# Kernel optimization log

Measured on AMD Instinct MI355X. Metric: run time of the kernel, lower is better.

## Reference

```python
import jax, jax.numpy as jnp
import numpy as np

N = 50000      # nodes
E = 800000     # edges (avg degree 16)
IN = 128       # in_channels
H = 8          # heads (layer 1)
C = 32         # hidden_channels per head
OUT = 40       # out_channels + 1
NEG_SLOPE = 0.2  # PyG GATConv default


def glorot(key, shape, fan_in, fan_out):
    lim = np.sqrt(6.0 / (fan_in + fan_out)).astype(np.float32)
    return jax.random.uniform(key, shape, jnp.float32, -lim, lim)


def setup_inputs() -> dict:
    key = jax.random.key(0)
    ks = jax.random.split(key, 10)
    x = jax.random.normal(ks[0], (N, IN), jnp.float32)
    edge_index = jax.random.randint(ks[1], (2, E), 0, N, dtype=jnp.int32)
    # layer 1: in -> H*C, heads=8, concat
    W1 = glorot(ks[2], (IN, H * C), IN, H * C)
    att_src1 = glorot(ks[3], (H, C), C, C)
    att_dst1 = glorot(ks[4], (H, C), C, C)
    b1 = jnp.zeros((H * C,), jnp.float32)
    # layer 2: H*C -> OUT, heads=1
    W2 = glorot(ks[5], (H * C, OUT), H * C, OUT)
    att_src2 = glorot(ks[6], (1, OUT), OUT, OUT)
    att_dst2 = glorot(ks[7], (1, OUT), OUT, OUT)
    b2 = jnp.zeros((OUT,), jnp.float32)
    return {"x": x, "edge_index": edge_index, "W1": W1, "att_src1": att_src1,
            "att_dst1": att_dst1, "b1": b1, "W2": W2, "att_src2": att_src2,
            "att_dst2": att_dst2, "b2": b2}


def gat_conv(x, edge_index, W, att_src, att_dst, bias):
    # PyG GATConv (eval mode, add_self_loops=True, concat=True)
    n = x.shape[0]
    heads, ch = att_src.shape
    loop = jnp.arange(n, dtype=edge_index.dtype)
    src = jnp.concatenate([edge_index[0], loop])  # message source j
    dst = jnp.concatenate([edge_index[1], loop])  # message target i
    h = (x @ W).reshape(n, heads, ch)                       # [N,H,C]
    a_src = jnp.einsum('nhc,hc->nh', h, att_src)            # [N,H]
    a_dst = jnp.einsum('nhc,hc->nh', h, att_dst)            # [N,H]
    logits = jax.nn.leaky_relu(a_src[src] + a_dst[dst], NEG_SLOPE)  # [Et,H]
    # segmented softmax over incoming edges of each target node
    m = jax.ops.segment_max(logits, dst, num_segments=n)    # [N,H]
    p = jnp.exp(logits - m[dst])
    s = jax.ops.segment_sum(p, dst, num_segments=n)         # [N,H]
    alpha = p / s[dst]                                      # [Et,H]
    msg = h[src] * alpha[:, :, None]                        # [Et,H,C]
    out = jax.ops.segment_sum(msg, dst, num_segments=n)     # [N,H,C]
    return out.reshape(n, heads * ch) + bias


def reference(x, edge_index, W1, att_src1, att_dst1, b1, W2, att_src2, att_dst2, b2):
    h = gat_conv(x, edge_index, W1, att_src1, att_dst1, b1)
    h = jax.nn.relu(h)  # dropout is identity in eval mode
    h = gat_conv(h, edge_index, W2, att_src2, att_dst2, b2)
    return jax.nn.log_softmax(h, axis=1)
```

## Files before the change

kernel.cpp:

```cpp
#include <hip/hip_runtime.h>
#include <hip/hip_bf16.h>
#include <math.h>

#define NEG_SLOPE 0.2f

__device__ __forceinline__ float lrelu(float x){ return x > 0.f ? x : NEG_SLOPE * x; }
__device__ __forceinline__ unsigned short f2bf(float f){
  __hip_bfloat16 h = __float2bfloat16(f);
  return __builtin_bit_cast(unsigned short, h);
}
__device__ __forceinline__ float b2f(unsigned short u){
  return __builtin_bit_cast(float, (unsigned)u << 16);
}

typedef short bf16x8 __attribute__((ext_vector_type(8)));
typedef float f32x4 __attribute__((ext_vector_type(4)));

__global__ void k_count(const int* __restrict__ dst, int* __restrict__ deg, int E){
  int e = blockIdx.x*256 + threadIdx.x;
  if (e < E) atomicAdd(&deg[dst[e]], 1);
}

__global__ __launch_bounds__(256) void k_scan1(const int* __restrict__ deg, int* __restrict__ bsum, int n){
  int tid = threadIdx.x;
  int base = blockIdx.x*1024 + tid*4;
  int s = 0;
  #pragma unroll
  for (int j=0;j<4;j++){ int idx = base+j; if (idx < n) s += deg[idx]; }
  #pragma unroll
  for (int off=32; off; off>>=1) s += __shfl_xor(s, off);
  __shared__ int ws[4];
  if ((tid&63)==0) ws[tid>>6] = s;
  __syncthreads();
  if (tid==0) bsum[blockIdx.x] = ws[0]+ws[1]+ws[2]+ws[3];
}

__global__ void k_scan2(const int* __restrict__ bsum, int* __restrict__ boff,
                        int* __restrict__ rowptr, int nb, int n){
  int lane = threadIdx.x;
  int v = (lane < nb) ? bsum[lane] : 0;
  int inc = v;
  #pragma unroll
  for (int off=1; off<64; off<<=1){ int t = __shfl_up(inc, off); if (lane >= off) inc += t; }
  if (lane < nb) boff[lane] = inc - v;
  if (lane == 63) rowptr[n] = inc;
}

__global__ __launch_bounds__(256) void k_scan3(const int* __restrict__ deg, const int* __restrict__ boff,
    int* __restrict__ rowptr, int* __restrict__ nxt, int n){
  int tid = threadIdx.x; int lane = tid & 63, w = tid >> 6;
  int base = blockIdx.x*1024 + tid*4;
  int v[4]; int s = 0;
  #pragma unroll
  for (int j=0;j<4;j++){ int idx = base+j; v[j] = (idx < n) ? deg[idx] : 0; s += v[j]; }
  int inc = s;
  #pragma unroll
  for (int off=1; off<64; off<<=1){ int t = __shfl_up(inc, off); if (lane >= off) inc += t; }
  __shared__ int ws[4];
  if (lane == 63) ws[w] = inc;
  __syncthreads();
  int run = boff[blockIdx.x];
  for (int ww=0; ww<w; ww++) run += ws[ww];
  run += inc - s;
  #pragma unroll
  for (int j=0;j<4;j++){ int idx = base+j; if (idx < n){ rowptr[idx] = run; nxt[idx] = run; run += v[j]; } }
}

__global__ void k_scatter(const int* __restrict__ src, const int* __restrict__ dst,
                          int* __restrict__ nxt, int* __restrict__ srcs,
                          int* __restrict__ dsts, int E){
  int e = blockIdx.x*256 + threadIdx.x;
  if (e < E){
    int d = dst[e];
    int pos = atomicAdd(&nxt[d], 1);
    srcs[pos] = src[e];
    dsts[pos] = d;
  }
}

__global__ void k_wt(const float* __restrict__ W, unsigned short* __restrict__ Wt, int NCreal){
  int c = blockIdx.x, k = threadIdx.x, K = blockDim.x;
  float v = (c < NCreal) ? W[(size_t)k*NCreal + c] : 0.f;
  Wt[(size_t)c*K + k] = f2bf(v);
}

__global__ void k_edgep1(const int* __restrict__ srcs, const int* __restrict__ dsts,
    const float* __restrict__ asrc, const float* __restrict__ adst,
    unsigned short* __restrict__ p1, int E8){
  int id = blockIdx.x*256 + threadIdx.x;
  if (id >= E8) return;
  int pos = id >> 3, hd = id & 7;
  int s = srcs[pos], d = dsts[pos];
  float l = lrelu(asrc[(size_t)s*8 + hd] + adst[(size_t)d*8 + hd]);
  p1[id] = f2bf(__expf(l));
}

__global__ void k_edgep2(const int* __restrict__ srcs, const int* __restrict__ dsts,
    const float* __restrict__ asrc, const float* __restrict__ adst,
    float* __restrict__ p2, int E){
  int pos = blockIdx.x*256 + threadIdx.x;
  if (pos >= E) return;
  int s = srcs[pos], d = dsts[pos];
  p2[pos] = __expf(lrelu(asrc[s] + adst[d]));
}

__global__ __launch_bounds__(256) void gemm1_att(
    const float* __restrict__ x, const unsigned short* __restrict__ Bt,
    unsigned short* __restrict__ C, const float* __restrict__ att_s,
    const float* __restrict__ att_d, float* __restrict__ asrc,
    float* __restrict__ adst, int M){
  __shared__ unsigned short sA[64][40];
  __shared__ unsigned short sB[256][40];
  const int tid = threadIdx.x;
  const int wid = tid >> 6, lane = tid & 63;
  const int r0 = blockIdx.x * 64;
  const int fr = lane & 15, fk = (lane >> 4) * 8;
  f32x4 acc[4][4] = {};

  for (int k0 = 0; k0 < 128; k0 += 32){
    #pragma unroll
    for (int t=0; t<2; t++){
      int id = tid + t*256;
      int r = id >> 3, q = id & 7;
      float4 v = make_float4(0.f,0.f,0.f,0.f);
      int row = r0 + r;
      if (row < M) v = ((const float4*)(x + (size_t)row*128))[(k0>>2) + q];
      ushort4 o; o.x=f2bf(v.x); o.y=f2bf(v.y); o.z=f2bf(v.z); o.w=f2bf(v.w);
      *(ushort4*)&sA[r][q*4] = o;
    }
    #pragma unroll
    for (int t=0; t<4; t++){
      int id = tid + t*256;
      int r = id >> 2, lk = (id & 3) * 8;
      uint4 vb = *(const uint4*)(Bt + (size_t)r*128 + k0 + lk);
      *(uint4*)&sB[r][lk] = vb;
    }
    __syncthreads();
    bf16x8 a[4], b[4];
    #pragma unroll
    for (int mi=0; mi<4; mi++) a[mi] = *(const bf16x8*)&sA[mi*16 + fr][fk];
    #pragma unroll
    for (int ni=0; ni<4; ni++) b[ni] = *(const bf16x8*)&sB[wid*64 + ni*16 + fr][fk];
    #pragma unroll
    for (int mi=0; mi<4; mi++)
      #pragma unroll
      for (int ni=0; ni<4; ni++)
        acc[mi][ni] = __builtin_amdgcn_mfma_f32_16x16x32_bf16(a[mi], b[ni], acc[mi][ni], 0,0,0);
    __syncthreads();
  }

  float avs[4], avd[4];
  #pragma unroll
  for (int ni=0; ni<4; ni++){
    int idx = (2*wid + (ni>>1))*32 + (ni&1)*16 + fr;
    avs[ni] = att_s[idx];
    avd[ni] = att_d[idx];
  }

  #pragma unroll
  for (int mi=0; mi<4; mi++){
    #pragma unroll
    for (int j=0; j<4; j++){
      int row = r0 + mi*16 + (lane>>4)*4 + j;
      #pragma unroll
      for (int ni=0; ni<4; ni++){
        int col = wid*64 + ni*16 + fr;
        if (row < M) C[(size_t)row*256 + col] = f2bf(acc[mi][ni][j]);
      }
      float s0 = acc[mi][0][j]*avs[0] + acc[mi][1][j]*avs[1];
      float s1 = acc[mi][2][j]*avs[2] + acc[mi][3][j]*avs[3];
      float d0 = acc[mi][0][j]*avd[0] + acc[mi][1][j]*avd[1];
      float d1 = acc[mi][2][j]*avd[2] + acc[mi][3][j]*avd[3];
      #pragma unroll
      for (int mk=1; mk<16; mk<<=1){
        s0 += __shfl_xor(s0, mk); s1 += __shfl_xor(s1, mk);
        d0 += __shfl_xor(d0, mk); d1 += __shfl_xor(d1, mk);
      }
      if ((lane & 15) == 0 && row < M){
        asrc[(size_t)row*8 + 2*wid    ] = s0;
        asrc[(size_t)row*8 + 2*wid + 1] = s1;
        adst[(size_t)row*8 + 2*wid    ] = d0;
        adst[(size_t)row*8 + 2*wid + 1] = d1;
      }
    }
  }
}

__global__ __launch_bounds__(256) void gemm_mfma(
    const unsigned short* __restrict__ A, const unsigned short* __restrict__ Bt,
    unsigned short* __restrict__ C, int M, int K, int ldc){
  __shared__ unsigned short sA[64][40];
  __shared__ unsigned short sB[64][40];
  const int tid = threadIdx.x;
  const int wid = tid >> 6, lane = tid & 63;
  const int r0 = blockIdx.x * 64, c0 = blockIdx.y * 64;
  const int wr = wid >> 1, wc = wid & 1;
  const int lr = tid >> 2;
  const int lk = (tid & 3) * 8;
  const int fr = lane & 15, fk = (lane >> 4) * 8;
  f32x4 acc[2][2] = {};

  for (int k0 = 0; k0 < K; k0 += 32){
    uint4 va = make_uint4(0,0,0,0);
    int row = r0 + lr;
    if (row < M) va = *(const uint4*)(A + (size_t)row*K + k0 + lk);
    *(uint4*)&sA[lr][lk] = va;
    uint4 vb = *(const uint4*)(Bt + (size_t)(c0 + lr)*K + k0 + lk);
    *(uint4*)&sB[lr][lk] = vb;
    __syncthreads();
    bf16x8 a0 = *(const bf16x8*)&sA[wr*32 + fr][fk];
    bf16x8 a1 = *(const bf16x8*)&sA[wr*32 + 16 + fr][fk];
    bf16x8 b0 = *(const bf16x8*)&sB[wc*32 + fr][fk];
    bf16x8 b1 = *(const bf16x8*)&sB[wc*32 + 16 + fr][fk];
    acc[0][0] = __builtin_amdgcn_mfma_f32_16x16x32_bf16(a0, b0, acc[0][0], 0,0,0);
    acc[0][1] = __builtin_amdgcn_mfma_f32_16x16x32_bf16(a0, b1, acc[0][1], 0,0,0);
    acc[1][0] = __builtin_amdgcn_mfma_f32_16x16x32_bf16(a1, b0, acc[1][0], 0,0,0);
    acc[1][1] = __builtin_amdgcn_mfma_f32_16x16x32_bf16(a1, b1, acc[1][1], 0,0,0);
    __syncthreads();
  }
  #pragma unroll
  for (int mi=0; mi<2; mi++){
    int rowb = r0 + wr*32 + mi*16 + (lane>>4)*4;
    #pragma unroll
    for (int ni=0; ni<2; ni++){
      int col = c0 + wc*32 + ni*16 + fr;
      #pragma unroll
      for (int j=0;j<4;j++){
        int row = rowb + j;
        if (row < M) C[(size_t)row*ldc + col] = f2bf(acc[mi][ni][j]);
      }
    }
  }
}

__global__ void k_att2(const unsigned short* __restrict__ h, const float* __restrict__ att_s,
    const float* __restrict__ att_d, float* __restrict__ asrc, float* __restrict__ adst, int n){
  int id = blockIdx.x*256 + threadIdx.x;
  if (id >= n) return;
  const unsigned short* hv = h + (size_t)id*64;
  float s = 0.f, d = 0.f;
  #pragma unroll
  for (int q=0; q<5; q++){
    ushort4 u0 = ((const ushort4*)hv)[q*2];
    ushort4 u1 = ((const ushort4*)hv)[q*2+1];
    float v0=b2f(u0.x), v1=b2f(u0.y), v2=b2f(u0.z), v3=b2f(u0.w);
    float v4=b2f(u1.x), v5=b2f(u1.y), v6=b2f(u1.z), v7=b2f(u1.w);
    float4 a0 = ((const float4*)att_s)[q*2], a1 = ((const float4*)att_s)[q*2+1];
    float4 d0 = ((const float4*)att_d)[q*2], d1 = ((const float4*)att_d)[q*2+1];
    s += v0*a0.x + v1*a0.y + v2*a0.z + v3*a0.w + v4*a1.x + v5*a1.y + v6*a1.z + v7*a1.w;
    d += v0*d0.x + v1*d0.y + v2*d0.z + v3*d0.w + v4*d1.x + v5*d1.y + v6*d1.z + v7*d1.w;
  }
  asrc[id] = s; adst[id] = d;
}

__global__ __launch_bounds__(256) void k_agg1(
    const unsigned short* __restrict__ h1, const float* __restrict__ asrc,
    const float* __restrict__ adst, const int* __restrict__ rowptr,
    const int* __restrict__ srcs, const unsigned short* __restrict__ p1,
    const float* __restrict__ bias, unsigned short* __restrict__ zb, int n){
  int i = (blockIdx.x*256 + threadIdx.x) >> 6;
  int lane = threadIdx.x & 63;
  if (i >= n) return;
  int hd = lane >> 3;
  float pself = __expf(lrelu(asrc[(size_t)i*8 + hd] + adst[(size_t)i*8 + hd]));
  float ssum = pself;
  uint2 hs = ((const uint2*)(h1 + (size_t)i*256))[lane];
  float4 acc;
  acc.x = pself * b2f((unsigned short)(hs.x & 0xffff));
  acc.y = pself * b2f((unsigned short)(hs.x >> 16));
  acc.z = pself * b2f((unsigned short)(hs.y & 0xffff));
  acc.w = pself * b2f((unsigned short)(hs.y >> 16));
  int e0 = rowptr[i], e1 = rowptr[i+1];
  int efull = e0 + ((e1 - e0) & ~7);
  for (int e = e0; e < efull; e += 8){
    int sx[8]; uint2 vv[8]; float pv[8];
    #pragma unroll
    for (int j=0;j<8;j++) sx[j] = srcs[e+j];
    #pragma unroll
    for (int j=0;j<8;j++) vv[j] = ((const uint2*)(h1 + (size_t)sx[j]*256))[lane];
    #pragma unroll
    for (int j=0;j<8;j++) pv[j] = b2f(p1[(size_t)(e+j)*8 + hd]);
    #pragma unroll
    for (int j=0;j<8;j++){
      float p = pv[j];
      ssum += p;
      acc.x += p * b2f((unsigned short)(vv[j].x & 0xffff));
      acc.y += p * b2f((unsigned short)(vv[j].x >> 16));
      acc.z += p * b2f((unsigned short)(vv[j].y & 0xffff));
      acc.w += p * b2f((unsigned short)(vv[j].y >> 16));
    }
  }
  if (efull < e1){
    int sx[8]; uint2 vv[8]; float pv[8];
    #pragma unroll
    for (int j=0;j<8;j++){
      int ee = efull + j;
      int idx = ee < e1 ? ee : e1 - 1;
      sx[j] = srcs[idx];
      unsigned short pr = p1[(size_t)idx*8 + hd];
      pv[j] = (ee < e1) ? b2f(pr) : 0.f;
    }
    #pragma unroll
    for (int j=0;j<8;j++) vv[j] = ((const uint2*)(h1 + (size_t)sx[j]*256))[lane];
    #pragma unroll
    for (int j=0;j<8;j++){
      float p = pv[j];
      ssum += p;
      acc.x += p * b2f((unsigned short)(vv[j].x & 0xffff));
      acc.y += p * b2f((unsigned short)(vv[j].x >> 16));
      acc.z += p * b2f((unsigned short)(vv[j].y & 0xffff));
      acc.w += p * b2f((unsigned short)(vv[j].y >> 16));
    }
  }
  float inv = 1.f / ssum;
  float4 b = ((const float4*)bias)[lane];
  ushort4 ob;
  ob.x = f2bf(fmaxf(fmaf(acc.x, inv, b.x), 0.f));
  ob.y = f2bf(fmaxf(fmaf(acc.y, inv, b.y), 0.f));
  ob.z = f2bf(fmaxf(fmaf(acc.z, inv, b.z), 0.f));
  ob.w = f2bf(fmaxf(fmaf(acc.w, inv, b.w), 0.f));
  ((ushort4*)(zb + (size_t)i*256))[lane] = ob;
}

__global__ __launch_bounds__(256) void k_agg2(
    const unsigned short* __restrict__ h2, const float* __restrict__ asrc,
    const float* __restrict__ adst, const int* __restrict__ rowptr,
    const int* __restrict__ srcs, const float* __restrict__ p2,
    const float* __restrict__ bias, float* __restrict__ out, int n){
  int wid = (blockIdx.x*256 + threadIdx.x) >> 6;
  int lane = threadIdx.x & 63;
  if (wid >= n) return;
  int i = wid;
  bool act = lane < 40;
  float pself = __expf(lrelu(asrc[i] + adst[i]));
  float ssum = pself;
  float acc = pself * b2f(h2[(size_t)i*64 + lane]);
  int e0 = rowptr[i], e1 = rowptr[i+1];
  int efull = e0 + ((e1 - e0) & ~7);
  for (int e = e0; e < efull; e += 8){
    int sx[8]; float vv[8], pv[8];
    #pragma unroll
    for (int j=0;j<8;j++) sx[j] = srcs[e+j];
    #pragma unroll
    for (int j=0;j<8;j++) vv[j] = b2f(h2[(size_t)sx[j]*64 + lane]);
    #pragma unroll
    for (int j=0;j<8;j++) pv[j] = p2[e+j];
    #pragma unroll
    for (int j=0;j<8;j++){
      ssum += pv[j];
      acc += pv[j] * vv[j];
    }
  }
  if (efull < e1){
    int sx[8]; float vv[8], pv[8];
    #pragma unroll
    for (int j=0;j<8;j++){
      int ee = efull + j;
      int idx = ee < e1 ? ee : e1 - 1;
      sx[j] = srcs[idx];
      float pr = p2[idx];
      pv[j] = (ee < e1) ? pr : 0.f;
    }
    #pragma unroll
    for (int j=0;j<8;j++) vv[j] = b2f(h2[(size_t)sx[j]*64 + lane]);
    #pragma unroll
    for (int j=0;j<8;j++){
      ssum += pv[j];
      acc += pv[j] * vv[j];
    }
  }
  float val = act ? (acc/ssum + bias[lane]) : -INFINITY;
  float mx = val;
  #pragma unroll
  for (int off=32; off; off>>=1) mx = fmaxf(mx, __shfl_xor(mx, off));
  float ex = act ? __expf(val - mx) : 0.f;
  float se = ex;
  #pragma unroll
  for (int off=32; off; off>>=1) se += __shfl_xor(se, off);
  if (act) out[(size_t)i*40 + lane] = val - mx - __logf(se);
}

extern "C" void kernel_launch(void* const* d_in, const int* in_sizes, int n_in,
                              void* d_out, int out_size, void* d_ws, size_t ws_size,
                              hipStream_t stream){
  const float* x   = (const float*)d_in[0];
  const int*   ei  = (const int*)d_in[1];
  const float* W1  = (const float*)d_in[2];
  const float* as1 = (const float*)d_in[3];
  const float* ad1 = (const float*)d_in[4];
  const float* b1  = (const float*)d_in[5];
  const float* W2  = (const float*)d_in[6];
  const float* as2 = (const float*)d_in[7];
  const float* ad2 = (const float*)d_in[8];
  const float* b2  = (const float*)d_in[9];
  float* out = (float*)d_out;

  const int N = in_sizes[0] / 128;
  const int E = in_sizes[1] / 2;
  const int* srcI = ei;
  const int* dstI = ei + E;

  char* ws = (char*)d_ws;
  size_t off = 0;
  auto alloc = [&](size_t bytes){ void* p = ws + off; off += (bytes + 255) & ~(size_t)255; return p; };
  unsigned short* h1b = (unsigned short*)alloc((size_t)N*256*2);
  unsigned short* zb  = (unsigned short*)alloc((size_t)N*256*2);
  unsigned short* h2b = (unsigned short*)alloc((size_t)N*64*2);
  unsigned short* W1t = (unsigned short*)alloc((size_t)256*128*2);
  unsigned short* W2t = (unsigned short*)alloc((size_t)64*256*2);
  unsigned short* p1  = (unsigned short*)alloc((size_t)E*8*2);
  float* p2    = (float*)alloc((size_t)E*4);
  float* asrc1 = (float*)alloc((size_t)N*8*4);
  float* adst1 = (float*)alloc((size_t)N*8*4);
  float* asrc2 = (float*)alloc((size_t)N*4);
  float* adst2 = (float*)alloc((size_t)N*4);
  int* deg     = (int*)alloc((size_t)N*4);
  int* rowptr  = (int*)alloc((size_t)(N+1)*4);
  int* nxt     = (int*)alloc((size_t)N*4);
  int* srcs    = (int*)alloc((size_t)E*4);
  int* dsts    = (int*)alloc((size_t)E*4);
  int* bsum    = (int*)alloc(256*4);
  int* boff    = (int*)alloc(256*4);
  (void)ws_size; (void)n_in; (void)out_size;

  const int nb = (N + 1023)/1024;
  hipMemsetAsync(deg, 0, (size_t)N*4, stream);
  int eb = (E + 255)/256;
  k_count <<<eb, 256, 0, stream>>>(dstI, deg, E);
  k_scan1 <<<nb, 256, 0, stream>>>(deg, bsum, N);
  k_scan2 <<<1, 64, 0, stream>>>(bsum, boff, rowptr, nb, N);
  k_scan3 <<<nb, 256, 0, stream>>>(deg, boff, rowptr, nxt, N);
  k_scatter<<<eb, 256, 0, stream>>>(srcI, dstI, nxt, srcs, dsts, E);

  k_wt <<<256, 128, 0, stream>>>(W1, W1t, 256);
  k_wt <<<64, 256, 0, stream>>>(W2, W2t, 40);

  gemm1_att<<<(N + 63)/64, 256, 0, stream>>>(x, W1t, h1b, as1, ad1, asrc1, adst1, N);
  k_edgep1<<<(E*8 + 255)/256, 256, 0, stream>>>(srcs, dsts, asrc1, adst1, p1, E*8);
  k_agg1<<<(N + 3)/4, 256, 0, stream>>>(h1b, asrc1, adst1, rowptr, srcs, p1, b1, zb, N);

  dim3 g2((N + 63)/64, 1);
  gemm_mfma<<<g2, 256, 0, stream>>>(zb, W2t, h2b, N, 256, 64);
  k_att2<<<(N + 255)/256, 256, 0, stream>>>(h2b, as2, ad2, asrc2, adst2, N);
  k_edgep2<<<eb, 256, 0, stream>>>(srcs, dsts, asrc2, adst2, p2, E);
  k_agg2<<<(N + 3)/4, 256, 0, stream>>>(h2b, asrc2, adst2, rowptr, srcs, p2, b2, out, N);
}
```

Measured before the change: 329.9 us.

## Fuse layer-2 attention logits into GEMM epilogue and split agg1 across two waves

Merges the two weight-transpose launches into one kernel. Folds the layer-2 attention dot products into the MFMA GEMM epilogue using shuffle reductions and a shared-memory combine, which removes the separate k_att2 pass over h2. Splits each layer-1 aggregation node across two wavefronts, each handling four heads with 32-bit loads, to raise parallelism and memory-level parallelism in the gather. The cost is twice as many waves re-reading srcs and rowptr per node, plus narrower per-lane loads.

```diff
diff --git a/kernel.cpp b/kernel.cpp
--- a/kernel.cpp
+++ b/kernel.cpp
@@ -78,10 +78,17 @@
   }
 }
 
-__global__ void k_wt(const float* __restrict__ W, unsigned short* __restrict__ Wt, int NCreal){
-  int c = blockIdx.x, k = threadIdx.x, K = blockDim.x;
-  float v = (c < NCreal) ? W[(size_t)k*NCreal + c] : 0.f;
-  Wt[(size_t)c*K + k] = f2bf(v);
+__global__ __launch_bounds__(256) void k_wt2(const float* __restrict__ W1, unsigned short* __restrict__ W1t,
+                                             const float* __restrict__ W2, unsigned short* __restrict__ W2t){
+  int b = blockIdx.x, tid = threadIdx.x;
+  if (b < 128){
+    int c = b*2 + (tid>>7), k = tid & 127;
+    W1t[(size_t)c*128 + k] = f2bf(W1[(size_t)k*256 + c]);
+  } else {
+    int c = b - 128, k = tid;
+    float v = (c < 40) ? W2[(size_t)k*40 + c] : 0.f;
+    W2t[(size_t)c*256 + k] = f2bf(v);
+  }
 }
 
 __global__ void k_edgep1(const int* __restrict__ srcs, const int* __restrict__ dsts,
@@ -186,18 +193,22 @@
   }
 }
 
-__global__ __launch_bounds__(256) void gemm_mfma(
+__global__ __launch_bounds__(256) void gemm2_att(
     const unsigned short* __restrict__ A, const unsigned short* __restrict__ Bt,
-    unsigned short* __restrict__ C, int M, int K, int ldc){
+    unsigned short* __restrict__ C, const float* __restrict__ att_s,
+    const float* __restrict__ att_d, float* __restrict__ asrc,
+    float* __restrict__ adst, int M){
   __shared__ unsigned short sA[64][40];
   __shared__ unsigned short sB[64][40];
+  __shared__ float sS[2][64], sD[2][64];
   const int tid = threadIdx.x;
   const int wid = tid >> 6, lane = tid & 63;
-  const int r0 = blockIdx.x * 64, c0 = blockIdx.y * 64;
+  const int r0 = blockIdx.x * 64;
   const int wr = wid >> 1, wc = wid & 1;
   const int lr = tid >> 2;
   const int lk = (tid & 3) * 8;
   const int fr = lane & 15, fk = (lane >> 4) * 8;
+  const int K = 256;
   f32x4 acc[2][2] = {};
 
   for (int k0 = 0; k0 < K; k0 += 32){
@@ -205,7 +216,7 @@
     int row = r0 + lr;
     if (row < M) va = *(const uint4*)(A + (size_t)row*K + k0 + lk);
     *(uint4*)&sA[lr][lk] = va;
-    uint4 vb = *(const uint4*)(Bt + (size_t)(c0 + lr)*K + k0 + lk);
+    uint4 vb = *(const uint4*)(Bt + (size_t)lr*K + k0 + lk);
     *(uint4*)&sB[lr][lk] = vb;
     __syncthreads();
     bf16x8 a0 = *(const bf16x8*)&sA[wr*32 + fr][fk];
@@ -218,39 +229,43 @@
     acc[1][1] = __builtin_amdgcn_mfma_f32_16x16x32_bf16(a1, b1, acc[1][1], 0,0,0);
     __syncthreads();
   }
+
+  float avs[2], avd[2];
+  #pragma unroll
+  for (int ni=0; ni<2; ni++){
+    int col = wc*32 + ni*16 + fr;
+    avs[ni] = (col < 40) ? att_s[col] : 0.f;
+    avd[ni] = (col < 40) ? att_d[col] : 0.f;
+  }
+
   #pragma unroll
   for (int mi=0; mi<2; mi++){
-    int rowb = r0 + wr*32 + mi*16 + (lane>>4)*4;
-    #pragma unroll
-    for (int ni=0; ni<2; ni++){
-      int col = c0 + wc*32 + ni*16 + fr;
+    #pragma unroll
+    for (int j=0;j<4;j++){
+      int lrow = wr*32 + mi*16 + (lane>>4)*4 + j;
+      int row = r0 + lrow;
       #pragma unroll
-      for (int j=0;j<4;j++){
-        int row = rowb + j;
-        if (row < M) C[(size_t)row*ldc + col] = f2bf(acc[mi][ni][j]);
+      for (int ni=0; ni<2; ni++){
+        int col = wc*32 + ni*16 + fr;
+        if (row < M) C[(size_t)row*64 + col] = f2bf(acc[mi][ni][j]);
       }
-    }
-  }
-}
-
-__global__ void k_att2(const unsigned short* __restrict__ h, const float* __restrict__ att_s,
-    const float* __restrict__ att_d, float* __restrict__ asrc, float* __restrict__ adst, int n){
-  int id = blockIdx.x*256 + threadIdx.x;
-  if (id >= n) return;
-  const unsigned short* hv = h + (size_t)id*64;
-  float s = 0.f, d = 0.f;
-  #pragma unroll
-  for (int q=0; q<5; q++){
-    ushort4 u0 = ((const ushort4*)hv)[q*2];
-    ushort4 u1 = ((const ushort4*)hv)[q*2+1];
-    float v0=b2f(u0.x), v1=b2f(u0.y), v2=b2f(u0.z), v3=b2f(u0.w);
-    float v4=b2f(u1.x), v5=b2f(u1.y), v6=b2f(u1.z), v7=b2f(u1.w);
-    float4 a0 = ((const float4*)att_s)[q*2], a1 = ((const float4*)att_s)[q*2+1];
-    float4 d0 = ((const float4*)att_d)[q*2], d1 = ((const float4*)att_d)[q*2+1];
-    s += v0*a0.x + v1*a0.y + v2*a0.z + v3*a0.w + v4*a1.x + v5*a1.y + v6*a1.z + v7*a1.w;
-    d += v0*d0.x + v1*d0.y + v2*d0.z + v3*d0.w + v4*d1.x + v5*d1.y + v6*d1.z + v7*d1.w;
-  }
-  asrc[id] = s; adst[id] = d;
+      float s = acc[mi][0][j]*avs[0] + acc[mi][1][j]*avs[1];
+      float d = acc[mi][0][j]*avd[0] + acc[mi][1][j]*avd[1];
+      #pragma unroll
+      for (int mk=1; mk<16; mk<<=1){
+        s += __shfl_xor(s, mk); d += __shfl_xor(d, mk);
+      }
+      if ((lane & 15) == 0){ sS[wc][lrow] = s; sD[wc][lrow] = d; }
+    }
+  }
+  __syncthreads();
+  if (tid < 64){
+    int row = r0 + tid;
+    if (row < M){
+      asrc[row] = sS[0][tid] + sS[1][tid];
+      adst[row] = sD[0][tid] + sD[1][tid];
+    }
+  }
 }
 
 __global__ __launch_bounds__(256) void k_agg1(
@@ -258,40 +273,36 @@
     const float* __restrict__ adst, const int* __restrict__ rowptr,
     const int* __restrict__ srcs, const unsigned short* __restrict__ p1,
     const float* __restrict__ bias, unsigned short* __restrict__ zb, int n){
-  int i = (blockIdx.x*256 + threadIdx.x) >> 6;
+  int gw = (blockIdx.x*256 + threadIdx.x) >> 6;
   int lane = threadIdx.x & 63;
+  int i = gw >> 1, half = gw & 1;
   if (i >= n) return;
-  int hd = lane >> 3;
+  int hd = half*4 + (lane >> 4);
   float pself = __expf(lrelu(asrc[(size_t)i*8 + hd] + adst[(size_t)i*8 + hd]));
   float ssum = pself;
-  uint2 hs = ((const uint2*)(h1 + (size_t)i*256))[lane];
-  float4 acc;
-  acc.x = pself * b2f((unsigned short)(hs.x & 0xffff));
-  acc.y = pself * b2f((unsigned short)(hs.x >> 16));
-  acc.z = pself * b2f((unsigned short)(hs.y & 0xffff));
-  acc.w = pself * b2f((unsigned short)(hs.y >> 16));
+  unsigned hv = ((const unsigned*)(h1 + (size_t)i*256))[half*64 + lane];
+  float accx = pself * b2f((unsigned short)(hv & 0xffff));
+  float accy = pself * b2f((unsigned short)(hv >> 16));
   int e0 = rowptr[i], e1 = rowptr[i+1];
   int efull = e0 + ((e1 - e0) & ~7);
   for (int e = e0; e < efull; e += 8){
-    int sx[8]; uint2 vv[8]; float pv[8];
+    int sx[8]; unsigned vv[8]; float pv[8];
     #pragma unroll
     for (int j=0;j<8;j++) sx[j] = srcs[e+j];
     #pragma unroll
-    for (int j=0;j<8;j++) vv[j] = ((const uint2*)(h1 + (size_t)sx[j]*256))[lane];
+    for (int j=0;j<8;j++) vv[j] = ((const unsigned*)(h1 + (size_t)sx[j]*256))[half*64 + lane];
     #pragma unroll
     for (int j=0;j<8;j++) pv[j] = b2f(p1[(size_t)(e+j)*8 + hd]);
     #pragma unroll
     for (int j=0;j<8;j++){
       float p = pv[j];
       ssum += p;
-      acc.x += p * b2f((unsigned short)(vv[j].x & 0xffff));
-      acc.y += p * b2f((unsigned short)(vv[j].x >> 16));
-      acc.z += p * b2f((unsigned short)(vv[j].y & 0xffff));
-      acc.w += p * b2f((unsigned short)(vv[j].y >> 16));
+      accx += p * b2f((unsigned short)(vv[j] & 0xffff));
+      accy += p * b2f((unsigned short)(vv[j] >> 16));
     }
   }
   if (efull < e1){
-    int sx[8]; uint2 vv[8]; float pv[8];
+    int sx[8]; unsigned vv[8]; float pv[8];
     #pragma unroll
     for (int j=0;j<8;j++){
       int ee = efull + j;
@@ -301,25 +312,20 @@
       pv[j] = (ee < e1) ? b2f(pr) : 0.f;
     }
     #pragma unroll
-    for (int j=0;j<8;j++) vv[j] = ((const uint2*)(h1 + (size_t)sx[j]*256))[lane];
+    for (int j=0;j<8;j++) vv[j] = ((const unsigned*)(h1 + (size_t)sx[j]*256))[half*64 + lane];
     #pragma unroll
     for (int j=0;j<8;j++){
       float p = pv[j];
       ssum += p;
-      acc.x += p * b2f((unsigned short)(vv[j].x & 0xffff));
-      acc.y += p * b2f((unsigned short)(vv[j].x >> 16));
-      acc.z += p * b2f((unsigned short)(vv[j].y & 0xffff));
-      acc.w += p * b2f((unsigned short)(vv[j].y >> 16));
+      accx += p * b2f((unsigned short)(vv[j] & 0xffff));
+      accy += p * b2f((unsigned short)(vv[j] >> 16));
     }
   }
   float inv = 1.f / ssum;
-  float4 b = ((const float4*)bias)[lane];
-  ushort4 ob;
-  ob.x = f2bf(fmaxf(fmaf(acc.x, inv, b.x), 0.f));
-  ob.y = f2bf(fmaxf(fmaf(acc.y, inv, b.y), 0.f));
-  ob.z = f2bf(fmaxf(fmaf(acc.z, inv, b.z), 0.f));
-  ob.w = f2bf(fmaxf(fmaf(acc.w, inv, b.w), 0.f));
-  ((ushort4*)(zb + (size_t)i*256))[lane] = ob;
+  float2 b = ((const float2*)bias)[half*64 + lane];
+  unsigned ob = (unsigned)f2bf(fmaxf(fmaf(accx, inv, b.x), 0.f))
+              | ((unsigned)f2bf(fmaxf(fmaf(accy, inv, b.y), 0.f)) << 16);
+  ((unsigned*)(zb + (size_t)i*256))[half*64 + lane] = ob;
 }
 
 __global__ __launch_bounds__(256) void k_agg2(
@@ -432,16 +438,13 @@
   k_scan3 <<<nb, 256, 0, stream>>>(deg, boff, rowptr, nxt, N);
   k_scatter<<<eb, 256, 0, stream>>>(srcI, dstI, nxt, srcs, dsts, E);
 
-  k_wt <<<256, 128, 0, stream>>>(W1, W1t, 256);
-  k_wt <<<64, 256, 0, stream>>>(W2, W2t, 40);
+  k_wt2<<<192, 256, 0, stream>>>(W1, W1t, W2, W2t);
 
   gemm1_att<<<(N + 63)/64, 256, 0, stream>>>(x, W1t, h1b, as1, ad1, asrc1, adst1, N);
   k_edgep1<<<(E*8 + 255)/256, 256, 0, stream>>>(srcs, dsts, asrc1, adst1, p1, E*8);
-  k_agg1<<<(N + 3)/4, 256, 0, stream>>>(h1b, asrc1, adst1, rowptr, srcs, p1, b1, zb, N);
-
-  dim3 g2((N + 63)/64, 1);
-  gemm_mfma<<<g2, 256, 0, stream>>>(zb, W2t, h2b, N, 256, 64);
-  k_att2<<<(N + 255)/256, 256, 0, stream>>>(h2b, as2, ad2, asrc2, adst2, N);
+  k_agg1<<<(2*N + 3)/4, 256, 0, stream>>>(h1b, asrc1, adst1, rowptr, srcs, p1, b1, zb, N);
+
+  gemm2_att<<<(N + 63)/64, 256, 0, stream>>>(zb, W2t, h2b, as2, ad2, asrc2, adst2, N);
   k_edgep2<<<eb, 256, 0, stream>>>(srcs, dsts, asrc2, adst2, p2, E);
   k_agg2<<<(N + 3)/4, 256, 0, stream>>>(h2b, asrc2, adst2, rowptr, srcs, p2, b2, out, N);
 }
```

New measurement: 337.1 us. 2.2% more time.
